# Optimization experiments

Measured on AMD Instinct MI355X. Metric: run time of the kernel, lower is better.

Reference implementation:

```python
import jax, jax.numpy as jnp
import numpy as np
import math

ALGEBRA_DIM = 32
HEAD_DIM = 128

def hadamard_matrix(n: int) -> jnp.ndarray:
    H = np.ones((1, 1), dtype=np.float32)
    while H.shape[0] < n:
        H = np.block([[H, H], [H, -H]])
    return jnp.asarray(H / math.sqrt(n))

def setup_inputs() -> dict:
    key = jax.random.key(0)
    kx, kw = jax.random.split(key)
    B, T, D = 4, 4096, HEAD_DIM
    x = jax.random.normal(kx, (B, ALGEBRA_DIM, T, D), dtype=jnp.float32)
    W = jax.random.normal(kw, (ALGEBRA_DIM, D, D), dtype=jnp.float32) * 0.02
    beta = jnp.full((D,), math.sqrt(3.0 / (2.0 * D)), dtype=jnp.float32)
    return {"x": x, "W": W, "beta": beta}

def reference(x, W, beta):
    # x: [B, 32, T, D]
    H = hadamard_matrix(ALGEBRA_DIM)  # [32, 32], orthonormal
    x_mixed = jnp.einsum('bhti,hg->bgti', x, H)       # Hadamard mix across heads
    y = jnp.einsum('bhti,hio->bhto', x_mixed, W)      # per-head DxD matmul
    y_mixed = jnp.einsum('bhti,hg->bgti', y, H)       # Hadamard mix again
    return y_mixed * beta                             # broadcast over last dim D
```

## Files before the change

kernel.cpp:

```cpp
#include <hip/hip_runtime.h>
#include <hip/hip_bf16.h>

#define NH 32
#define D_ 128
#define TT 16
#define B_ 4
#define T_ 4096

typedef short bf16x8 __attribute__((ext_vector_type(8)));
typedef float f32x4  __attribute__((ext_vector_type(4)));
typedef unsigned int u32;
typedef unsigned short u16;

__device__ __forceinline__ u16 f2bf(float f) {
    u32 x = __builtin_bit_cast(u32, f);
    u32 r = (x + 0x7FFFu + ((x >> 16) & 1u)) >> 16;
    return (u16)r;
}

__global__ void k0_wprep(const float* __restrict__ W, uint4* __restrict__ Wf) {
    int gid  = blockIdx.x * blockDim.x + threadIdx.x;
    int lane = gid & 63;
    int kt   = (gid >> 6) & 3;
    int nt   = (gid >> 8) & 7;
    int h    = gid >> 11;
    int o     = nt * 16 + (lane & 15);
    int ibase = kt * 32 + (lane >> 4) * 8;
    u16 v[8];
#pragma unroll
    for (int j = 0; j < 8; ++j)
        v[j] = f2bf(W[((size_t)h * D_ + (ibase + j)) * D_ + o]);
    uint4 o4;
    o4.x = (u32)v[0] | ((u32)v[1] << 16);
    o4.y = (u32)v[2] | ((u32)v[3] << 16);
    o4.z = (u32)v[4] | ((u32)v[5] << 16);
    o4.w = (u32)v[6] | ((u32)v[7] << 16);
    Wf[gid] = o4;
}

__global__ __launch_bounds__(512, 1)
void k1_mix_gemm(const float* __restrict__ x, const uint4* __restrict__ Wf,
                 u16* __restrict__ y, int tile0) {
    __shared__ u16 slab[NH * TT * D_];
    char* sb = (char*)slab;

    int tile = tile0 + blockIdx.x;
    int b  = tile >> 8;
    int t0 = (tile & 255) * TT;
    int tid = threadIdx.x;

    {
        int iop  = tid & 63;
        int trow = tid >> 6;
#pragma unroll
        for (int pass = 0; pass < 2; ++pass) {
            int t = pass * 8 + trow;
            const float* src = x + ((size_t)(b * NH) * T_ + (t0 + t)) * D_ + iop * 2;
            float2 v[NH];
#pragma unroll
            for (int h = 0; h < NH; ++h)
                v[h] = *(const float2*)(src + (size_t)h * T_ * D_);
#pragma unroll
            for (int s = 1; s < NH; s <<= 1) {
#pragma unroll
                for (int j = 0; j < NH; ++j) {
                    if (j & s) continue;
                    float2 a = v[j], c = v[j + s];
                    v[j]     = make_float2(a.x + c.x, a.y + c.y);
                    v[j + s] = make_float2(a.x - c.x, a.y - c.y);
                }
            }
            u32 base = ((u32)(t * 256 + iop * 4)) ^ (((u32)t & 7u) << 4);
#pragma unroll
            for (int h = 0; h < NH; ++h) {
                u32 p = (u32)f2bf(v[h].x) | ((u32)f2bf(v[h].y) << 16);
                *(u32*)(sb + h * 4096 + base) = p;
            }
        }
    }
    __syncthreads();

    int lane = tid & 63;
    int w    = tid >> 6;
    int ta   = lane & 15;
    int kg   = lane >> 4;
    size_t ytile = (size_t)blockIdx.x * NH * TT * D_;

#pragma unroll 2
    for (int h = 0; h < NH; ++h) {
        f32x4 acc = {0.f, 0.f, 0.f, 0.f};
        const uint4* wfp = Wf + (((size_t)h * 8 + w) * 4) * 64 + lane;
#pragma unroll
        for (int kc = 0; kc < 4; ++kc) {
            u32 abyte = ((u32)(ta * 256 + (kc * 32 + kg * 8) * 2)) ^ (((u32)ta & 7u) << 4);
            bf16x8 a = *(const bf16x8*)(sb + h * 4096 + abyte);
            bf16x8 bb = __builtin_bit_cast(bf16x8, wfp[(size_t)kc * 64]);
            acc = __builtin_amdgcn_mfma_f32_16x16x32_bf16(a, bb, acc, 0, 0, 0);
        }
        int o = w * 16 + (lane & 15);
        size_t yb = ytile + (size_t)h * TT * D_;
#pragma unroll
        for (int r = 0; r < 4; ++r) {
            int t = kg * 4 + r;
            y[yb + t * D_ + o] = f2bf(acc[r]);
        }
    }
}

__global__ __launch_bounds__(256, 1)
void k2_mix_beta(const u16* __restrict__ y, const float* __restrict__ beta,
                 float* __restrict__ out, int tile0) {
    int tile = tile0 + blockIdx.x;
    int b  = tile >> 8;
    int t0 = (tile & 255) * TT;
    int tid = threadIdx.x;
    int op = tid & 63;
    int tq = tid >> 6;

    float2 bv = *(const float2*)(beta + op * 2);
    float s0 = bv.x * (1.0f / 32.0f);
    float s1 = bv.y * (1.0f / 32.0f);

    const u16* yb = y + (size_t)blockIdx.x * NH * TT * D_;
#pragma unroll
    for (int ti = 0; ti < 4; ++ti) {
        int t = tq * 4 + ti;
        float2 v[NH];
#pragma unroll
        for (int h = 0; h < NH; ++h) {
            u32 p = *(const u32*)(yb + (h * TT + t) * D_ + op * 2);
            v[h].x = __builtin_bit_cast(float, p << 16);
            v[h].y = __builtin_bit_cast(float, p & 0xFFFF0000u);
        }
#pragma unroll
        for (int s = 1; s < NH; s <<= 1) {
#pragma unroll
            for (int j = 0; j < NH; ++j) {
                if (j & s) continue;
                float2 a = v[j], c = v[j + s];
                v[j]     = make_float2(a.x + c.x, a.y + c.y);
                v[j + s] = make_float2(a.x - c.x, a.y - c.y);
            }
        }
#pragma unroll
        for (int g = 0; g < NH; ++g) {
            float2 o2 = make_float2(v[g].x * s0, v[g].y * s1);
            *(float2*)(out + ((size_t)(b * NH + g) * T_ + (t0 + t)) * D_ + op * 2) = o2;
        }
    }
}

extern "C" void kernel_launch(void* const* d_in, const int* in_sizes, int n_in,
                              void* d_out, int out_size, void* d_ws, size_t ws_size,
                              hipStream_t stream) {
    const float* x    = (const float*)d_in[0];
    const float* W    = (const float*)d_in[1];
    const float* beta = (const float*)d_in[2];
    float* out = (float*)d_out;

    size_t wf_bytes = (size_t)NH * D_ * D_ * 2;
    uint4* Wf = (uint4*)d_ws;
    u16* ybuf = (u16*)((char*)d_ws + wf_bytes);
    size_t avail = (ws_size > wf_bytes) ? ws_size - wf_bytes : 0;

    const int total_tiles = B_ * (T_ / TT);
    size_t per_tile = (size_t)NH * TT * D_ * 2;
    int tiles_per_chunk = (int)(avail / per_tile);
    if (tiles_per_chunk > total_tiles) tiles_per_chunk = total_tiles;
    if (tiles_per_chunk < 1) tiles_per_chunk = 1;

    k0_wprep<<<256, 256, 0, stream>>>(W, Wf);
    for (int t0 = 0; t0 < total_tiles; t0 += tiles_per_chunk) {
        int n = total_tiles - t0;
        if (n > tiles_per_chunk) n = tiles_per_chunk;
        k1_mix_gemm<<<n, 512, 0, stream>>>(x, Wf, ybuf, t0);
        k2_mix_beta<<<n, 256, 0, stream>>>(ybuf, beta, out, t0);
    }
}
```

Baseline: 530.7 us.

## Fuse GEMM and second Hadamard mix into one kernel, keep accumulators in registers

Measured after the change: 477.4 us. -10.0%, faster.

```diff
diff --git a/kernel.cpp b/kernel.cpp
--- a/kernel.cpp
+++ b/kernel.cpp
@@ -38,44 +38,42 @@
     Wf[gid] = o4;
 }
 
-__global__ __launch_bounds__(512, 1)
-void k1_mix_gemm(const float* __restrict__ x, const uint4* __restrict__ Wf,
-                 u16* __restrict__ y, int tile0) {
+__global__ __launch_bounds__(512, 2)
+void k_fused(const float* __restrict__ x, const uint4* __restrict__ Wf,
+             const float* __restrict__ beta, float* __restrict__ out) {
     __shared__ u16 slab[NH * TT * D_];
     char* sb = (char*)slab;
 
-    int tile = tile0 + blockIdx.x;
+    int tile = blockIdx.x;
     int b  = tile >> 8;
     int t0 = (tile & 255) * TT;
     int tid = threadIdx.x;
 
     {
-        int iop  = tid & 63;
-        int trow = tid >> 6;
+        int ifour = tid & 31;
+        int t     = tid >> 5;
+        const float* src = x + ((size_t)(b * NH) * T_ + (t0 + t)) * D_ + ifour * 4;
+        f32x4 v[NH];
 #pragma unroll
-        for (int pass = 0; pass < 2; ++pass) {
-            int t = pass * 8 + trow;
-            const float* src = x + ((size_t)(b * NH) * T_ + (t0 + t)) * D_ + iop * 2;
-            float2 v[NH];
+        for (int h = 0; h < NH; ++h)
+            v[h] = *(const f32x4*)(src + (size_t)h * T_ * D_);
 #pragma unroll
-            for (int h = 0; h < NH; ++h)
-                v[h] = *(const float2*)(src + (size_t)h * T_ * D_);
+        for (int s = 1; s < NH; s <<= 1) {
 #pragma unroll
-            for (int s = 1; s < NH; s <<= 1) {
+            for (int j = 0; j < NH; ++j) {
+                if (j & s) continue;
+                f32x4 a = v[j], c = v[j + s];
+                v[j]     = a + c;
+                v[j + s] = a - c;
+            }
+        }
+        u32 base = ((u32)(t * 256 + ifour * 8)) ^ (((u32)t & 7u) << 4);
 #pragma unroll
-                for (int j = 0; j < NH; ++j) {
-                    if (j & s) continue;
-                    float2 a = v[j], c = v[j + s];
-                    v[j]     = make_float2(a.x + c.x, a.y + c.y);
-                    v[j + s] = make_float2(a.x - c.x, a.y - c.y);
-                }
-            }
-            u32 base = ((u32)(t * 256 + iop * 4)) ^ (((u32)t & 7u) << 4);
-#pragma unroll
-            for (int h = 0; h < NH; ++h) {
-                u32 p = (u32)f2bf(v[h].x) | ((u32)f2bf(v[h].y) << 16);
-                *(u32*)(sb + h * 4096 + base) = p;
-            }
+        for (int h = 0; h < NH; ++h) {
+            uint2 p;
+            p.x = (u32)f2bf(v[h][0]) | ((u32)f2bf(v[h][1]) << 16);
+            p.y = (u32)f2bf(v[h][2]) | ((u32)f2bf(v[h][3]) << 16);
+            *(uint2*)(sb + h * 4096 + base) = p;
         }
     }
     __syncthreads();
@@ -84,69 +82,43 @@
     int w    = tid >> 6;
     int ta   = lane & 15;
     int kg   = lane >> 4;
-    size_t ytile = (size_t)blockIdx.x * NH * TT * D_;
 
-#pragma unroll 2
+    f32x4 acc[NH];
+#pragma unroll
+    for (int h = 0; h < NH; ++h) acc[h] = f32x4{0.f, 0.f, 0.f, 0.f};
+
+#pragma unroll
     for (int h = 0; h < NH; ++h) {
-        f32x4 acc = {0.f, 0.f, 0.f, 0.f};
         const uint4* wfp = Wf + (((size_t)h * 8 + w) * 4) * 64 + lane;
 #pragma unroll
         for (int kc = 0; kc < 4; ++kc) {
             u32 abyte = ((u32)(ta * 256 + (kc * 32 + kg * 8) * 2)) ^ (((u32)ta & 7u) << 4);
-            bf16x8 a = *(const bf16x8*)(sb + h * 4096 + abyte);
+            bf16x8 a  = *(const bf16x8*)(sb + h * 4096 + abyte);
             bf16x8 bb = __builtin_bit_cast(bf16x8, wfp[(size_t)kc * 64]);
-            acc = __builtin_amdgcn_mfma_f32_16x16x32_bf16(a, bb, acc, 0, 0, 0);
-        }
-        int o = w * 16 + (lane & 15);
-        size_t yb = ytile + (size_t)h * TT * D_;
-#pragma unroll
-        for (int r = 0; r < 4; ++r) {
-            int t = kg * 4 + r;
-            y[yb + t * D_ + o] = f2bf(acc[r]);
+            acc[h] = __builtin_amdgcn_mfma_f32_16x16x32_bf16(a, bb, acc[h], 0, 0, 0);
         }
     }
-}
 
-__global__ __launch_bounds__(256, 1)
-void k2_mix_beta(const u16* __restrict__ y, const float* __restrict__ beta,
-                 float* __restrict__ out, int tile0) {
-    int tile = tile0 + blockIdx.x;
-    int b  = tile >> 8;
-    int t0 = (tile & 255) * TT;
-    int tid = threadIdx.x;
-    int op = tid & 63;
-    int tq = tid >> 6;
+#pragma unroll
+    for (int s = 1; s < NH; s <<= 1) {
+#pragma unroll
+        for (int j = 0; j < NH; ++j) {
+            if (j & s) continue;
+            f32x4 a = acc[j], c = acc[j + s];
+            acc[j]     = a + c;
+            acc[j + s] = a - c;
+        }
+    }
 
-    float2 bv = *(const float2*)(beta + op * 2);
-    float s0 = bv.x * (1.0f / 32.0f);
-    float s1 = bv.y * (1.0f / 32.0f);
-
-    const u16* yb = y + (size_t)blockIdx.x * NH * TT * D_;
+    int o = w * 16 + ta;
+    float bv = beta[o] * (1.0f / 32.0f);
+    float* op0 = out + ((size_t)b * NH * T_ + (t0 + kg * 4)) * D_ + o;
 #pragma unroll
-    for (int ti = 0; ti < 4; ++ti) {
-        int t = tq * 4 + ti;
-        float2 v[NH];
+    for (int g = 0; g < NH; ++g) {
+        float* og = op0 + (size_t)g * T_ * D_;
 #pragma unroll
-        for (int h = 0; h < NH; ++h) {
-            u32 p = *(const u32*)(yb + (h * TT + t) * D_ + op * 2);
-            v[h].x = __builtin_bit_cast(float, p << 16);
-            v[h].y = __builtin_bit_cast(float, p & 0xFFFF0000u);
-        }
-#pragma unroll
-        for (int s = 1; s < NH; s <<= 1) {
-#pragma unroll
-            for (int j = 0; j < NH; ++j) {
-                if (j & s) continue;
-                float2 a = v[j], c = v[j + s];
-                v[j]     = make_float2(a.x + c.x, a.y + c.y);
-                v[j + s] = make_float2(a.x - c.x, a.y - c.y);
-            }
-        }
-#pragma unroll
-        for (int g = 0; g < NH; ++g) {
-            float2 o2 = make_float2(v[g].x * s0, v[g].y * s1);
-            *(float2*)(out + ((size_t)(b * NH + g) * T_ + (t0 + t)) * D_ + op * 2) = o2;
-        }
+        for (int r = 0; r < 4; ++r)
+            og[r * D_] = acc[g][r] * bv;
     }
 }
 
@@ -158,22 +130,8 @@
     const float* beta = (const float*)d_in[2];
     float* out = (float*)d_out;
 
-    size_t wf_bytes = (size_t)NH * D_ * D_ * 2;
     uint4* Wf = (uint4*)d_ws;
-    u16* ybuf = (u16*)((char*)d_ws + wf_bytes);
-    size_t avail = (ws_size > wf_bytes) ? ws_size - wf_bytes : 0;
-
-    const int total_tiles = B_ * (T_ / TT);
-    size_t per_tile = (size_t)NH * TT * D_ * 2;
-    int tiles_per_chunk = (int)(avail / per_tile);
-    if (tiles_per_chunk > total_tiles) tiles_per_chunk = total_tiles;
-    if (tiles_per_chunk < 1) tiles_per_chunk = 1;
 
     k0_wprep<<<256, 256, 0, stream>>>(W, Wf);
-    for (int t0 = 0; t0 < total_tiles; t0 += tiles_per_chunk) {
-        int n = total_tiles - t0;
-        if (n > tiles_per_chunk) n = tiles_per_chunk;
-        k1_mix_gemm<<<n, 512, 0, stream>>>(x, Wf, ybuf, t0);
-        k2_mix_beta<<<n, 256, 0, stream>>>(ybuf, beta, out, t0);
-    }
+    k_fused<<<B_ * (T_ / TT), 512, 0, stream>>>(x, Wf, beta, out);
 }
```
